# Performance work log

Hardware: AMD Instinct MI355X
Metric: run time of the kernel (lower is better)

Reference implementation:

```python
import jax, jax.numpy as jnp
import numpy as np

B, N, C, K, TOPK = 16, 4096, 256, 8, 2
EPS = 1e-6
RATIO = 0.1      # gate_geno_ratio
TEMP = 1.0       # gate_temperature


def setup_inputs() -> dict:
    key = jax.random.key(0)
    ks = jax.random.split(key, 8)
    s = np.float32(1.0 / np.sqrt(C))  # ~xavier scale for C->C linears
    return {
        "tokens": jax.random.normal(ks[0], (B, N, C), jnp.float32),
        "geno_vec": jax.random.normal(ks[1], (B, C), jnp.float32),
        # gate params (gate_proj init std=0.001; gate_geno given small random instead of exact-zero init so it contributes)
        "Wg": jax.random.normal(ks[2], (K, C), jnp.float32) * 0.001,
        "bg": jnp.zeros((K,), jnp.float32),
        "Wgg": jax.random.normal(ks[3], (K, C), jnp.float32) * 0.001,
        "bgg": jnp.zeros((K,), jnp.float32),
        # per-expert 2-layer MLP params (dropout inactive in eval)
        "W1": jax.random.normal(ks[4], (K, C, C), jnp.float32) * s,
        "b1": jnp.zeros((K, C), jnp.float32),
        "W2": jax.random.normal(ks[5], (K, C, C), jnp.float32) * s,
        "b2": jnp.zeros((K, C), jnp.float32),
    }


def reference(tokens, geno_vec, Wg, bg, Wgg, bgg, W1, b1, W2, b2):
    # gate logits: [B,N,K]
    logits = jnp.einsum("bnc,kc->bnk", tokens, Wg) + bg
    logits = logits + RATIO * (geno_vec @ Wgg.T + bgg)[:, None, :]
    logits = logits / TEMP

    topv, topi = jax.lax.top_k(logits, TOPK)          # [B,N,TOPK]
    topw = jax.nn.softmax(topv, axis=-1)
    topw = jnp.maximum(topw, EPS)
    topw = topw / topw.sum(-1, keepdims=True)

    # dense gate weight matrix W: [B,N,K] (scatter of topw at topi; topk indices are distinct)
    hot = jax.nn.one_hot(topi, K, dtype=tokens.dtype)  # [B,N,TOPK,K]
    Wmat = (hot * topw[..., None]).sum(-2)             # [B,N,K]

    # load-balance loss on hard usage (detached in original)
    usage = jax.lax.stop_gradient(hot.sum(-2).mean((0, 1)))  # [K]
    lb_loss = (jnp.std(usage) / (usage.mean() + EPS)) ** 2

    mass_sum = Wmat.sum(axis=1)                        # [B,K]

    # per-expert MLP computed densely over all tokens; zero gate weight kills
    # non-routed tokens exactly (same math as gather->MLP->scatter-add)
    def expert_center(k):
        h = jax.nn.relu(tokens @ W1[k].T + b1[k])      # [B,N,C]
        out = h @ W2[k].T + b2[k]                      # [B,N,C]
        return jnp.einsum("bn,bnc->bc", Wmat[:, :, k], out)

    centers_sum = jnp.stack([expert_center(k) for k in range(K)], axis=1)  # [B,K,C]
    centers = centers_sum / jnp.maximum(mass_sum, EPS)[..., None]

    routing_confidence = (topv[:, :, 0] - topv[:, :, 1]).mean()
    return centers, lb_loss, routing_confidence
```

## Files before the change

### kernel.cpp

```cpp
#include <hip/hip_runtime.h>

#define B_ 16
#define N_ 4096
#define C_ 256
#define K_ 8
#define EPS 1e-6f
#define RATIO 0.1f

typedef float f32x4 __attribute__((ext_vector_type(4)));
typedef __bf16 bf16x8 __attribute__((ext_vector_type(8)));

__device__ inline unsigned short f2bf(float f){
  unsigned int u = __float_as_uint(f);
  u += 0x7FFFu + ((u >> 16) & 1u);
  return (unsigned short)(u >> 16);
}
__device__ inline float bf2f(unsigned short h){
  return __uint_as_float(((unsigned int)h) << 16);
}

union BFu { ushort4 u4[2]; bf16x8 v; };

__global__ __launch_bounds__(256) void k0_prep(
    const float* __restrict__ W1, const float* __restrict__ Wg,
    const float* __restrict__ geno, const float* __restrict__ Wgg,
    const float* __restrict__ bgg,
    unsigned short* __restrict__ W1swz,
    unsigned short* __restrict__ Wgp_hi, unsigned short* __restrict__ Wgp_lo,
    int* __restrict__ cnt,
    float* __restrict__ mass, float* __restrict__ conf,
    float* __restrict__ glog)
{
  int gid = blockIdx.x * 256 + threadIdx.x;
  if (gid < B_*K_) { cnt[gid] = 0; mass[gid] = 0.f; }
  if (gid == 0) conf[0] = 0.f;
  {
    int o = gid << 3;
    int lane6 = (o >> 3) & 63;
    int s  = (o >> 9) & 7;
    int nt = (o >> 12) & 15;
    int k  = o >> 16;
    int quad = lane6 >> 4, l16 = lane6 & 15;
    int j  = nt*16 + l16;
    int c0 = s*32 + quad*8;
    const float* src = W1 + (k << 16) + (j << 8) + c0;
    unsigned short* dst = W1swz + o;
    #pragma unroll
    for (int e = 0; e < 8; ++e) dst[e] = f2bf(src[e]);
  }
  if (gid < 16*C_){
    int r = gid >> 8, c = gid & 255;
    float v = (r < K_) ? Wg[(r << 8) + c] : 0.f;
    unsigned short h = f2bf(v);
    Wgp_hi[gid] = h;
    Wgp_lo[gid] = f2bf(v - bf2f(h));
  }
  int wv = gid >> 6;
  if (wv < B_*K_){
    int lane = threadIdx.x & 63;
    int b = wv >> 3, k = wv & 7;
    float4 a = *(const float4*)(geno + b*C_ + lane*4);
    float4 w = *(const float4*)(Wgg  + k*C_ + lane*4);
    float p = a.x*w.x + a.y*w.y + a.z*w.z + a.w*w.w;
    #pragma unroll
    for (int off = 32; off; off >>= 1) p += __shfl_xor(p, off);
    if (lane == 0) glog[wv] = RATIO * (p + bgg[k]);
  }
}

__global__ __launch_bounds__(256) void k1_gate(
    const float* __restrict__ tokens,
    const unsigned short* __restrict__ Wgp_hi, const unsigned short* __restrict__ Wgp_lo,
    const float* __restrict__ bg, const float* __restrict__ glog,
    int* __restrict__ cnt, int* __restrict__ bidx, float* __restrict__ bw,
    float* __restrict__ mass, float* __restrict__ conf,
    unsigned short* __restrict__ tok_bf)
{
  __shared__ float ls[64][9];
  __shared__ float bg_s[K_], gl_s[K_], mass_s[K_];
  __shared__ int lcnt[K_], gbase[K_];
  __shared__ int e0s[64], e1s[64], s0s[64], s1s[64];
  __shared__ float w0s[64], w1s[64];
  int tid = threadIdx.x, lane = tid & 63, wave = tid >> 6;
  int quad = lane >> 4, l16 = lane & 15;
  int b = blockIdx.x >> 6;
  int tok0 = (blockIdx.x & 63) * 64;
  if (tid < K_){ bg_s[tid] = bg[tid]; gl_s[tid] = glog[b*K_ + tid];
                 mass_s[tid] = 0.f; lcnt[tid] = 0; }
  __syncthreads();

  {
    int trow = tok0 + wave*16 + l16;
    const float* xsrc = tokens + ((size_t)b*N_ + trow)*C_ + quad*8;
    unsigned short* bdst = tok_bf + (((size_t)(b*N_ + trow)) << 8) + quad*8;
    f32x4 acc; acc.x = 0.f; acc.y = 0.f; acc.z = 0.f; acc.w = 0.f;
    #pragma unroll
    for (int s = 0; s < 8; ++s){
      float4 xa = *(const float4*)(xsrc + s*32);
      float4 xb = *(const float4*)(xsrc + s*32 + 4);
      BFu hi, lo;
      hi.u4[0].x = f2bf(xa.x); hi.u4[0].y = f2bf(xa.y);
      hi.u4[0].z = f2bf(xa.z); hi.u4[0].w = f2bf(xa.w);
      hi.u4[1].x = f2bf(xb.x); hi.u4[1].y = f2bf(xb.y);
      hi.u4[1].z = f2bf(xb.z); hi.u4[1].w = f2bf(xb.w);
      lo.u4[0].x = f2bf(xa.x - bf2f(hi.u4[0].x));
      lo.u4[0].y = f2bf(xa.y - bf2f(hi.u4[0].y));
      lo.u4[0].z = f2bf(xa.z - bf2f(hi.u4[0].z));
      lo.u4[0].w = f2bf(xa.w - bf2f(hi.u4[0].w));
      lo.u4[1].x = f2bf(xb.x - bf2f(hi.u4[1].x));
      lo.u4[1].y = f2bf(xb.y - bf2f(hi.u4[1].y));
      lo.u4[1].z = f2bf(xb.z - bf2f(hi.u4[1].z));
      lo.u4[1].w = f2bf(xb.w - bf2f(hi.u4[1].w));
      *(ushort4*)(bdst + s*32)     = hi.u4[0];
      *(ushort4*)(bdst + s*32 + 4) = hi.u4[1];
      bf16x8 bhi = *(const bf16x8*)(Wgp_hi + l16*C_ + s*32 + quad*8);
      bf16x8 blo = *(const bf16x8*)(Wgp_lo + l16*C_ + s*32 + quad*8);
      acc = __builtin_amdgcn_mfma_f32_16x16x32_bf16(hi.v, bhi, acc, 0, 0, 0);
      acc = __builtin_amdgcn_mfma_f32_16x16x32_bf16(lo.v, bhi, acc, 0, 0, 0);
      acc = __builtin_amdgcn_mfma_f32_16x16x32_bf16(hi.v, blo, acc, 0, 0, 0);
    }
    if (l16 < K_){
      #pragma unroll
      for (int rr = 0; rr < 4; ++rr){
        int tl = wave*16 + quad*4 + rr;
        ls[tl][l16] = acc[rr] + bg_s[l16] + gl_s[l16];
      }
    }
  }
  __syncthreads();

  if (tid < 64){
    int t = tid;
    float v0 = -1e30f, v1 = -1e30f; int i0 = 0, i1 = 0;
    #pragma unroll
    for (int kk = 0; kk < K_; ++kk){
      float l = ls[t][kk];
      if (l > v0){ v1 = v0; i1 = i0; v0 = l; i0 = kk; }
      else if (l > v1){ v1 = l; i1 = kk; }
    }
    float e  = expf(v1 - v0);
    float w0 = 1.f / (1.f + e), w1 = e / (1.f + e);
    w0 = fmaxf(w0, EPS); w1 = fmaxf(w1, EPS);
    float inv = 1.f / (w0 + w1);
    w0 *= inv; w1 *= inv;
    int p0 = atomicAdd(&lcnt[i0], 1);
    int p1 = atomicAdd(&lcnt[i1], 1);
    e0s[t] = i0; e1s[t] = i1; s0s[t] = p0; s1s[t] = p1;
    w0s[t] = w0; w1s[t] = w1;
    atomicAdd(&mass_s[i0], w0);
    atomicAdd(&mass_s[i1], w1);
    float ca = v0 - v1;
    #pragma unroll
    for (int off = 32; off; off >>= 1) ca += __shfl_down(ca, off);
    if (t == 0) atomicAdd(conf, ca);
  }
  __syncthreads();
  if (tid < K_){
    gbase[tid] = atomicAdd(&cnt[b*K_ + tid], lcnt[tid]);
    atomicAdd(&mass[b*K_ + tid], mass_s[tid]);
  }
  __syncthreads();
  if (tid < 64){
    int t = tid;
    int n = tok0 + t;
    int ke0 = e0s[t], ke1 = e1s[t];
    size_t o0 = (size_t)(b*K_ + ke0)*N_ + gbase[ke0] + s0s[t];
    size_t o1 = (size_t)(b*K_ + ke1)*N_ + gbase[ke1] + s1s[t];
    bidx[o0] = n;  bw[o0] = w0s[t];
    bidx[o1] = n;  bw[o1] = w1s[t];
  }
}

__global__ __launch_bounds__(256, 4) void k4_expert(
    const unsigned short* __restrict__ tok_bf, const unsigned short* __restrict__ W1swz,
    const float* __restrict__ b1, const int* __restrict__ cnt,
    const int* __restrict__ bidx, const float* __restrict__ bw,
    float* __restrict__ gpart)
{
  int lin = blockIdx.x;
  int w = (lin & 7) * 512 + (lin >> 3);
  int bat = w >> 8;
  int k = (w >> 5) & 7;
  int chunk = w & 31;
  int bucket = (bat << 3) | k;
  int M = cnt[bucket];
  if (chunk * 128 >= M) return;
  int Mm1 = M - 1;

  __shared__ unsigned short Bs[4][4096];
  __shared__ float wtok[128];
  __shared__ float red[2][4][16];

  int tid = threadIdx.x, lane = tid & 63, wave = tid >> 6;
  int quad = lane >> 4, l16 = lane & 15;
  int bwbase = bucket << 12;

  const unsigned short* wsrc = W1swz + ((size_t)k << 16);

  #pragma unroll
  for (int pp = 0; pp < 2; ++pp){
    #pragma unroll
    for (int i = 0; i < 2; ++i){
      int c16 = pp*512 + i*256 + tid;
      __builtin_amdgcn_global_load_lds(
        (const __attribute__((address_space(1))) unsigned int*)(wsrc + c16*8),
        (__attribute__((address_space(3))) unsigned int*)(&Bs[pp][0] + (i*256 + tid)*8),
        16, 0, 0);
    }
  }

  if (tid < 128){
    int tn = chunk*128 + tid;
    wtok[tid] = (tn < M) ? bw[bwbase + tn] : 0.f;
  }

  int r0 = chunk*128 + (wave << 4) + l16;
  int nn0 = bidx[bwbase + min(r0, Mm1)];
  int nn1 = bidx[bwbase + min(r0 + 64, Mm1)];
  const unsigned short* p0 = tok_bf + (((size_t)((bat << 12) + nn0)) << 8) + (quad << 3);
  const unsigned short* p1 = tok_bf + (((size_t)((bat << 12) + nn1)) << 8) + (quad << 3);
  bf16x8 a0[8], a1[8];
  #pragma unroll
  for (int s = 0; s < 8; ++s){
    a0[s] = *(const bf16x8*)(p0 + s*32);
    a1[s] = *(const bf16x8*)(p1 + s*32);
  }

  float bias[16];
  #pragma unroll
  for (int p = 0; p < 16; ++p) bias[p] = b1[(k << 8) + (p << 4) + l16];

  float* gdst = gpart + (size_t)(((bucket << 5) + chunk) << 8);
  int wq = (wave << 4) + (quad << 2);

  #pragma unroll
  for (int p = 0; p < 16; ++p){
    if (p < 14){
      #pragma unroll
      for (int i = 0; i < 2; ++i){
        int c16 = (p + 2)*512 + i*256 + tid;
        __builtin_amdgcn_global_load_lds(
          (const __attribute__((address_space(1))) unsigned int*)(wsrc + c16*8),
          (__attribute__((address_space(3))) unsigned int*)(&Bs[(p + 2) & 3][0] + (i*256 + tid)*8),
          16, 0, 0);
      }
      asm volatile("s_waitcnt vmcnt(4) lgkmcnt(0)" ::: "memory");
    } else if (p == 14){
      asm volatile("s_waitcnt vmcnt(2) lgkmcnt(0)" ::: "memory");
    } else {
      asm volatile("s_waitcnt vmcnt(0) lgkmcnt(0)" ::: "memory");
    }
    __builtin_amdgcn_s_barrier();

    if (p > 0 && tid < 16){
      int pb = (p - 1) & 1;
      float sv = red[pb][0][tid] + red[pb][1][tid]
               + red[pb][2][tid] + red[pb][3][tid];
      gdst[((p - 1) << 4) + tid] = sv;
    }

    f32x4 acc0, acc1;
    acc0.x=0.f; acc0.y=0.f; acc0.z=0.f; acc0.w=0.f;
    acc1.x=0.f; acc1.y=0.f; acc1.z=0.f; acc1.w=0.f;
    #pragma unroll
    for (int s = 0; s < 8; ++s){
      bf16x8 bb = *(const bf16x8*)(&Bs[p & 3][0] + ((s*64 + lane) << 3));
      acc0 = __builtin_amdgcn_mfma_f32_16x16x32_bf16(a0[s], bb, acc0, 0, 0, 0);
      acc1 = __builtin_amdgcn_mfma_f32_16x16x32_bf16(a1[s], bb, acc1, 0, 0, 0);
    }
    float pt = 0.f;
    #pragma unroll
    for (int rr = 0; rr < 4; ++rr){
      float h0 = fmaxf(acc0[rr] + bias[p], 0.f);
      float h1 = fmaxf(acc1[rr] + bias[p], 0.f);
      pt += wtok[wq + rr] * h0 + wtok[64 + wq + rr] * h1;
    }
    pt += __shfl_down(pt, 32);
    pt += __shfl_down(pt, 16);
    if (lane < 16) red[p & 1][wave][lane] = pt;
  }
  asm volatile("s_waitcnt lgkmcnt(0)" ::: "memory");
  __builtin_amdgcn_s_barrier();
  if (tid < 16){
    float sv = red[1][0][tid] + red[1][1][tid] + red[1][2][tid] + red[1][3][tid];
    gdst[(15 << 4) + tid] = sv;
  }
}

__global__ __launch_bounds__(256) void k5_centers(
    const float* __restrict__ gpart, const int* __restrict__ cnt,
    const float* __restrict__ W2, const float* __restrict__ b2,
    const float* __restrict__ mass, const float* __restrict__ conf,
    float* __restrict__ out)
{
  __shared__ float gv[C_];
  int z = blockIdx.x, tid = threadIdx.x;
  int k = z & 7;
  int nch = (cnt[z] + 127) >> 7;
  float sv = 0.f;
  for (int c = 0; c < nch; ++c)
    sv += gpart[(size_t)((((z << 5) + c) << 8) + tid)];
  gv[tid] = sv;
  __syncthreads();
  float m = mass[z];
  float inv = 1.f / fmaxf(m, EPS);
  int tq = tid & 3, cb = tid >> 2;
  #pragma unroll 1
  for (int h = 0; h < 2; ++h){
    int c = (blockIdx.y*2 + h)*64 + cb;
    const float4* wrow = (const float4*)(W2 + ((((k << 8) + c)) << 8));
    float dot = 0.f;
    #pragma unroll
    for (int jj = 0; jj < 16; ++jj){
      float4 w4 = wrow[jj*4 + tq];
      float4 g4 = *(const float4*)&gv[(jj*4 + tq) * 4];
      dot += w4.x*g4.x + w4.y*g4.y + w4.z*g4.z + w4.w*g4.w;
    }
    dot += __shfl_xor(dot, 1);
    dot += __shfl_xor(dot, 2);
    if (tq == 0) out[z*C_ + c] = (dot + m * b2[k*C_ + c]) * inv;
  }
  if (z == 0 && blockIdx.y == 0 && tid == 0){
    float u[K_];
    #pragma unroll
    for (int kk = 0; kk < K_; ++kk) u[kk] = 0.f;
    for (int i = 0; i < B_*K_; ++i) u[i & 7] += (float)cnt[i];
    float mean = 0.f;
    #pragma unroll
    for (int kk = 0; kk < K_; ++kk){ u[kk] *= (1.f / (float)(B_*N_)); mean += u[kk]; }
    mean *= (1.f / K_);
    float var = 0.f;
    #pragma unroll
    for (int kk = 0; kk < K_; ++kk){ float d = u[kk] - mean; var += d*d; }
    var *= (1.f / K_);
    float denom = mean + EPS;
    out[B_*K_*C_]     = var / (denom * denom);
    out[B_*K_*C_ + 1] = conf[0] / (float)(B_*N_);
  }
}

extern "C" void kernel_launch(void* const* d_in, const int* in_sizes, int n_in,
                              void* d_out, int out_size, void* d_ws, size_t ws_size,
                              hipStream_t stream)
{
  const float* tokens = (const float*)d_in[0];
  const float* geno   = (const float*)d_in[1];
  const float* Wg     = (const float*)d_in[2];
  const float* bg     = (const float*)d_in[3];
  const float* Wgg    = (const float*)d_in[4];
  const float* bgg    = (const float*)d_in[5];
  const float* W1     = (const float*)d_in[6];
  const float* b1     = (const float*)d_in[7];
  const float* W2     = (const float*)d_in[8];
  const float* b2     = (const float*)d_in[9];
  float* out = (float*)d_out;
  char* ws = (char*)d_ws;
  unsigned short* W1swz  = (unsigned short*)(ws);
  unsigned short* Wgp_hi = (unsigned short*)(ws + 1048576);
  unsigned short* Wgp_lo = (unsigned short*)(ws + 1056768);
  float* glog = (float*)(ws + 1196032);
  int*   cnt  = (int*)  (ws + 1196544);
  float* mass = (float*)(ws + 1197056);
  float* conf = (float*)(ws + 1197568);
  int*   bidx = (int*)  (ws + 1198080);
  float* bw   = (float*)(ws + 3295232);
  unsigned short* tok_bf = (unsigned short*)(ws + 5392384);
  float* gpart = (float*)(ws + 38946816);

  k0_prep<<<256, 256, 0, stream>>>(W1, Wg, geno, Wgg, bgg, W1swz, Wgp_hi, Wgp_lo,
                                   cnt, mass, conf, glog);
  k1_gate<<<1024, 256, 0, stream>>>(tokens, Wgp_hi, Wgp_lo, bg, glog,
                                    cnt, bidx, bw, mass, conf, tok_bf);
  k4_expert<<<4096, 256, 0, stream>>>(tok_bf, W1swz, b1, cnt, bidx, bw, gpart);
  k5_centers<<<dim3(128, 2), 256, 0, stream>>>(gpart, cnt, W2, b2, mass, conf, out);
}
```

Baseline: 180.1 us.

## Deepen expert weight prefetch pipeline and batch gate token loads

The expert kernel's LDS weight ring grows from four to six stages with three tiles in flight, and the waitcnt thresholds are adjusted to match. The block-to-work mapping changes to interleave experts within halves of the grid, and launch bounds drop to three blocks per CU to fit the larger LDS footprint. In the gate kernel, all token loads are issued before the conversion and MFMA loop, top-k work is spread across four waves, and the confidence sum is reduced per wave before a single atomic. The aim is to hide global-load latency behind compute, at the cost of lower occupancy and more registers.

Result: no change. 181.4 us (+0.8%).

```diff
diff --git a/kernel.cpp b/kernel.cpp
--- a/kernel.cpp
+++ b/kernel.cpp
@@ -81,6 +81,7 @@
   __shared__ int lcnt[K_], gbase[K_];
   __shared__ int e0s[64], e1s[64], s0s[64], s1s[64];
   __shared__ float w0s[64], w1s[64];
+  __shared__ float cred[4];
   int tid = threadIdx.x, lane = tid & 63, wave = tid >> 6;
   int quad = lane >> 4, l16 = lane & 15;
   int b = blockIdx.x >> 6;
@@ -93,24 +94,28 @@
     int trow = tok0 + wave*16 + l16;
     const float* xsrc = tokens + ((size_t)b*N_ + trow)*C_ + quad*8;
     unsigned short* bdst = tok_bf + (((size_t)(b*N_ + trow)) << 8) + quad*8;
+    float4 xa[8], xb[8];
+    #pragma unroll
+    for (int s = 0; s < 8; ++s){
+      xa[s] = *(const float4*)(xsrc + s*32);
+      xb[s] = *(const float4*)(xsrc + s*32 + 4);
+    }
     f32x4 acc; acc.x = 0.f; acc.y = 0.f; acc.z = 0.f; acc.w = 0.f;
     #pragma unroll
     for (int s = 0; s < 8; ++s){
-      float4 xa = *(const float4*)(xsrc + s*32);
-      float4 xb = *(const float4*)(xsrc + s*32 + 4);
       BFu hi, lo;
-      hi.u4[0].x = f2bf(xa.x); hi.u4[0].y = f2bf(xa.y);
-      hi.u4[0].z = f2bf(xa.z); hi.u4[0].w = f2bf(xa.w);
-      hi.u4[1].x = f2bf(xb.x); hi.u4[1].y = f2bf(xb.y);
-      hi.u4[1].z = f2bf(xb.z); hi.u4[1].w = f2bf(xb.w);
-      lo.u4[0].x = f2bf(xa.x - bf2f(hi.u4[0].x));
-      lo.u4[0].y = f2bf(xa.y - bf2f(hi.u4[0].y));
-      lo.u4[0].z = f2bf(xa.z - bf2f(hi.u4[0].z));
-      lo.u4[0].w = f2bf(xa.w - bf2f(hi.u4[0].w));
-      lo.u4[1].x = f2bf(xb.x - bf2f(hi.u4[1].x));
-      lo.u4[1].y = f2bf(xb.y - bf2f(hi.u4[1].y));
-      lo.u4[1].z = f2bf(xb.z - bf2f(hi.u4[1].z));
-      lo.u4[1].w = f2bf(xb.w - bf2f(hi.u4[1].w));
+      hi.u4[0].x = f2bf(xa[s].x); hi.u4[0].y = f2bf(xa[s].y);
+      hi.u4[0].z = f2bf(xa[s].z); hi.u4[0].w = f2bf(xa[s].w);
+      hi.u4[1].x = f2bf(xb[s].x); hi.u4[1].y = f2bf(xb[s].y);
+      hi.u4[1].z = f2bf(xb[s].z); hi.u4[1].w = f2bf(xb[s].w);
+      lo.u4[0].x = f2bf(xa[s].x - bf2f(hi.u4[0].x));
+      lo.u4[0].y = f2bf(xa[s].y - bf2f(hi.u4[0].y));
+      lo.u4[0].z = f2bf(xa[s].z - bf2f(hi.u4[0].z));
+      lo.u4[0].w = f2bf(xa[s].w - bf2f(hi.u4[0].w));
+      lo.u4[1].x = f2bf(xb[s].x - bf2f(hi.u4[1].x));
+      lo.u4[1].y = f2bf(xb[s].y - bf2f(hi.u4[1].y));
+      lo.u4[1].z = f2bf(xb[s].z - bf2f(hi.u4[1].z));
+      lo.u4[1].w = f2bf(xb[s].w - bf2f(hi.u4[1].w));
       *(ushort4*)(bdst + s*32)     = hi.u4[0];
       *(ushort4*)(bdst + s*32 + 4) = hi.u4[1];
       bf16x8 bhi = *(const bf16x8*)(Wgp_hi + l16*C_ + s*32 + quad*8);
@@ -129,8 +134,8 @@
   }
   __syncthreads();
 
-  if (tid < 64){
-    int t = tid;
+  if (quad == 0){
+    int t = (wave << 4) | l16;
     float v0 = -1e30f, v1 = -1e30f; int i0 = 0, i1 = 0;
     #pragma unroll
     for (int kk = 0; kk < K_; ++kk){
@@ -151,17 +156,18 @@
     atomicAdd(&mass_s[i1], w1);
     float ca = v0 - v1;
     #pragma unroll
-    for (int off = 32; off; off >>= 1) ca += __shfl_down(ca, off);
-    if (t == 0) atomicAdd(conf, ca);
+    for (int off = 8; off; off >>= 1) ca += __shfl_down(ca, off);
+    if (l16 == 0) cred[wave] = ca;
   }
   __syncthreads();
   if (tid < K_){
     gbase[tid] = atomicAdd(&cnt[b*K_ + tid], lcnt[tid]);
     atomicAdd(&mass[b*K_ + tid], mass_s[tid]);
   }
-  __syncthreads();
-  if (tid < 64){
-    int t = tid;
+  if (tid == 0) atomicAdd(conf, cred[0] + cred[1] + cred[2] + cred[3]);
+  __syncthreads();
+  if (quad == 0){
+    int t = (wave << 4) | l16;
     int n = tok0 + t;
     int ke0 = e0s[t], ke1 = e1s[t];
     size_t o0 = (size_t)(b*K_ + ke0)*N_ + gbase[ke0] + s0s[t];
@@ -171,14 +177,27 @@
   }
 }
 
-__global__ __launch_bounds__(256, 4) void k4_expert(
+#define K4_STAGE(T, REG) do {                                                  \
+    _Pragma("unroll")                                                          \
+    for (int i = 0; i < 2; ++i){                                               \
+      int c16 = (T)*512 + i*256 + tid;                                         \
+      __builtin_amdgcn_global_load_lds(                                        \
+        (const __attribute__((address_space(1))) unsigned int*)(wsrc + c16*8), \
+        (__attribute__((address_space(3))) unsigned int*)(&Bs[REG][0] + (i*256 + tid)*8), \
+        16, 0, 0);                                                             \
+    }                                                                          \
+  } while(0)
+
+__global__ __launch_bounds__(256, 3) void k4_expert(
     const unsigned short* __restrict__ tok_bf, const unsigned short* __restrict__ W1swz,
     const float* __restrict__ b1, const int* __restrict__ cnt,
     const int* __restrict__ bidx, const float* __restrict__ bw,
     float* __restrict__ gpart)
 {
   int lin = blockIdx.x;
-  int w = (lin & 7) * 512 + (lin >> 3);
+  int halfg = lin >> 11;
+  int l2i = lin & 2047;
+  int w = (halfg << 11) | ((l2i & 7) << 8) | (l2i >> 3);
   int bat = w >> 8;
   int k = (w >> 5) & 7;
   int chunk = w & 31;
@@ -187,7 +206,7 @@
   if (chunk * 128 >= M) return;
   int Mm1 = M - 1;
 
-  __shared__ unsigned short Bs[4][4096];
+  __shared__ unsigned short Bs[6][4096];
   __shared__ float wtok[128];
   __shared__ float red[2][4][16];
 
@@ -197,17 +216,9 @@
 
   const unsigned short* wsrc = W1swz + ((size_t)k << 16);
 
-  #pragma unroll
-  for (int pp = 0; pp < 2; ++pp){
-    #pragma unroll
-    for (int i = 0; i < 2; ++i){
-      int c16 = pp*512 + i*256 + tid;
-      __builtin_amdgcn_global_load_lds(
-        (const __attribute__((address_space(1))) unsigned int*)(wsrc + c16*8),
-        (__attribute__((address_space(3))) unsigned int*)(&Bs[pp][0] + (i*256 + tid)*8),
-        16, 0, 0);
-    }
-  }
+  K4_STAGE(0, 0);
+  K4_STAGE(1, 1);
+  K4_STAGE(2, 2);
 
   if (tid < 128){
     int tn = chunk*128 + tid;
@@ -235,15 +246,10 @@
 
   #pragma unroll
   for (int p = 0; p < 16; ++p){
-    if (p < 14){
-      #pragma unroll
-      for (int i = 0; i < 2; ++i){
-        int c16 = (p + 2)*512 + i*256 + tid;
-        __builtin_amdgcn_global_load_lds(
-          (const __attribute__((address_space(1))) unsigned int*)(wsrc + c16*8),
-          (__attribute__((address_space(3))) unsigned int*)(&Bs[(p + 2) & 3][0] + (i*256 + tid)*8),
-          16, 0, 0);
-      }
+    if (p <= 12) K4_STAGE(p + 3, (p + 3) % 6);
+    if (p <= 12){
+      asm volatile("s_waitcnt vmcnt(6) lgkmcnt(0)" ::: "memory");
+    } else if (p == 13){
       asm volatile("s_waitcnt vmcnt(4) lgkmcnt(0)" ::: "memory");
     } else if (p == 14){
       asm volatile("s_waitcnt vmcnt(2) lgkmcnt(0)" ::: "memory");
@@ -264,7 +270,7 @@
     acc1.x=0.f; acc1.y=0.f; acc1.z=0.f; acc1.w=0.f;
     #pragma unroll
     for (int s = 0; s < 8; ++s){
-      bf16x8 bb = *(const bf16x8*)(&Bs[p & 3][0] + ((s*64 + lane) << 3));
+      bf16x8 bb = *(const bf16x8*)(&Bs[p % 6][0] + ((s*64 + lane) << 3));
       acc0 = __builtin_amdgcn_mfma_f32_16x16x32_bf16(a0[s], bb, acc0, 0, 0, 0);
       acc1 = __builtin_amdgcn_mfma_f32_16x16x32_bf16(a1[s], bb, acc1, 0, 0, 0);
     }
```
